# Performance work log

Measured on AMD Instinct MI355X. Metric: run time of the kernel, lower is better.

Reference implementation:

```python
import jax, jax.numpy as jnp
import numpy as np

T, D, H, FF, L = 4096, 512, 8, 2048, 6  # tokens, model dim, heads, ffn hidden, shared layers
HW = D // H  # head width = 64
N_SEG = 8
EPS = 1e-12


def setup_inputs() -> dict:
    key = jax.random.key(0)
    ks = jax.random.split(key, 16)
    s = 0.02

    def w(k, shape):
        return (jax.random.normal(k, shape, jnp.float32) * s)

    return {
        "h": jax.random.normal(ks[0], (T, D), jnp.float32),
        "seg_ids": jnp.sort(jax.random.randint(ks[1], (T,), 0, N_SEG, jnp.int32)),
        # attention projections (shared across layers, as in the torch module)
        "Wq": w(ks[2], (D, D)), "bq": jnp.zeros((D,), jnp.float32),
        "Wk": w(ks[3], (D, D)), "bk": jnp.zeros((D,), jnp.float32),
        "Wv": w(ks[4], (D, D)), "bv": jnp.zeros((D,), jnp.float32),
        "Wc": w(ks[5], (D, D)), "bc": jnp.zeros((D,), jnp.float32),
        # output projection
        "Wp": w(ks[6], (D, D)), "bp": jnp.zeros((D,), jnp.float32),
        # layer norms
        "g1": jnp.ones((D,), jnp.float32), "b1": jnp.zeros((D,), jnp.float32),
        "g2": jnp.ones((D,), jnp.float32), "b2": jnp.zeros((D,), jnp.float32),
        # position-wise FFN
        "W1": w(ks[7], (D, FF)), "fb1": jnp.zeros((FF,), jnp.float32),
        "W2": w(ks[8], (FF, D)), "fb2": jnp.zeros((D,), jnp.float32),
    }


def _layernorm(x, gamma, beta):
    # TF-style LN: eps inside the sqrt, biased variance
    u = x.mean(-1, keepdims=True)
    s = ((x - u) ** 2).mean(-1, keepdims=True)
    return gamma * (x - u) / jnp.sqrt(s + EPS) + beta


def _swish(x):
    return x * jax.nn.sigmoid(x)


def reference(h, seg_ids, Wq, bq, Wk, bk, Wv, bv, Wc, bc, Wp, bp,
              g1, b1, g2, b2, W1, fb1, W2, fb2):
    # Segment-local attention: equivalent to the torch per-split loop, since
    # softmax over a block-diagonal mask == per-segment softmax.
    mask = seg_ids[:, None] == seg_ids[None, :]  # [T, T]
    scale = 1.0 / np.sqrt(HW).astype(np.float32)
    for _ in range(L):  # shared weights across layers, as in the module
        prev = h
        q = (h @ Wq + bq).reshape(T, H, HW)
        k = (h @ Wk + bk).reshape(T, H, HW)
        v = (h @ Wv + bv).reshape(T, H, HW)
        c = h @ Wc + bc
        scores = jnp.einsum("thw,shw->hts", q, k) * scale  # [H, T, T]
        scores = jnp.where(mask[None], scores, jnp.float32(-1e30))
        att = jax.nn.softmax(scores, axis=-1)
        attn_out = jnp.einsum("hts,shw->thw", att, v).reshape(T, D) + c
        h = _layernorm(prev + attn_out @ Wp + bp, g1, b1)
        h = _layernorm(h + _swish(h @ W1 + fb1) @ W2 + fb2, g2, b2)
    return h
```

## Files before the change

### kernel.cpp

```cpp
#include <hip/hip_runtime.h>
#include <stdint.h>

#define TTOK 4096
#define DMODEL 512
#define NHEAD 8
#define FFDIM 2048
#define NLAYER 6

typedef short bf16x8 __attribute__((ext_vector_type(8)));
typedef float f32x4 __attribute__((ext_vector_type(4)));

__device__ __forceinline__ unsigned short f2bf(float f) {
  union { float f; unsigned int u; } v; v.f = f;
  unsigned int u = v.u;
  unsigned int r = (u + 0x7FFFu + ((u >> 16) & 1u)) >> 16;
  return (unsigned short)r;
}

__device__ __forceinline__ float bf2f(unsigned short h) {
  union { unsigned int u; float f; } v; v.u = ((unsigned int)h) << 16;
  return v.f;
}

#define GLOAD_LDS16(gp, lp)                                                      \
  __builtin_amdgcn_global_load_lds(                                              \
      (const __attribute__((address_space(1))) unsigned int*)(gp),               \
      (__attribute__((address_space(3))) unsigned int*)(lp), 16, 0, 0)

__global__ void transpose_cast(const float* __restrict__ src, unsigned short* __restrict__ dst,
                               int K, int N) {
  __shared__ float tile[32][33];
  const int n0 = blockIdx.x * 32, k0 = blockIdx.y * 32;
  const int x = threadIdx.x, y = threadIdx.y;
#pragma unroll
  for (int yy = 0; yy < 32; yy += 8)
    tile[y + yy][x] = src[(size_t)(k0 + y + yy) * N + n0 + x];
  __syncthreads();
#pragma unroll
  for (int yy = 0; yy < 32; yy += 8)
    dst[(size_t)(n0 + y + yy) * K + k0 + x] = f2bf(tile[x][y + yy]);
}

__global__ void pack_bias(const float* __restrict__ bq, const float* __restrict__ bk,
                          const float* __restrict__ bv, const float* __restrict__ bc,
                          float* __restrict__ out) {
  int i = blockIdx.x * 256 + threadIdx.x;
  const float* src = (i < 512) ? bq : (i < 1024) ? bk : (i < 1536) ? bv : bc;
  out[i] = src[i & 511];
}

__global__ void cast_bf16(const float* __restrict__ src, unsigned short* __restrict__ dst, int n4) {
  int i = blockIdx.x * 256 + threadIdx.x;
  if (i < n4) {
    float4 v = ((const float4*)src)[i];
    uint2 o;
    o.x = (unsigned int)f2bf(v.x) | ((unsigned int)f2bf(v.y) << 16);
    o.y = (unsigned int)f2bf(v.z) | ((unsigned int)f2bf(v.w) << 16);
    ((uint2*)dst)[i] = o;
  }
}

__global__ void seg_bounds(const int* __restrict__ seg, int* __restrict__ ss,
                           int* __restrict__ se, int T) {
  const int t = blockIdx.x * 256 + threadIdx.x;
  if (t >= T) return;
  const int sid = seg[t];
  int lo = 0, hi = T;
  while (lo < hi) { int mid = (lo + hi) >> 1; if (seg[mid] < sid) lo = mid + 1; else hi = mid; }
  ss[t] = lo;
  lo = t; hi = T;
  while (lo < hi) { int mid = (lo + hi) >> 1; if (seg[mid] <= sid) lo = mid + 1; else hi = mid; }
  se[t] = lo;
}

template <int MODE, int MF>
__launch_bounds__(256)
__global__ void gemm_bf16(const unsigned short* __restrict__ A,
                          const unsigned short* __restrict__ Bt,
                          int M, int N, int K,
                          const float* __restrict__ bias,
                          const float* __restrict__ res,
                          float* __restrict__ outF,
                          unsigned short* __restrict__ outB) {
  __shared__ uint4 As[MF * 256];
  __shared__ uint4 Bs[1024];
  const int tid = threadIdx.x;
  const int lane = tid & 63;
  const int wv = tid >> 6;
  const int wm = wv >> 1, wn = wv & 1;
  const int l15 = lane & 15, l4 = lane >> 4;
  const int bm0 = blockIdx.x * (MF * 32);
  const int bn0 = blockIdx.y * 128;

  f32x4 acc[MF][4];
#pragma unroll
  for (int m = 0; m < MF; ++m)
#pragma unroll
    for (int n = 0; n < 4; ++n) acc[m][n] = (f32x4){0.f, 0.f, 0.f, 0.f};

  for (int k0 = 0; k0 < K; k0 += 64) {
#pragma unroll
    for (int i = 0; i < MF; ++i) {
      const int u = tid + i * 256;
      const int r = u >> 3;
      const int c = (u & 7) ^ (r & 7);
      GLOAD_LDS16(A + (size_t)(bm0 + r) * K + k0 + c * 8, &As[i * 256 + wv * 64]);
    }
#pragma unroll
    for (int i = 0; i < 4; ++i) {
      const int u = tid + i * 256;
      const int r = u >> 3;
      const int c = (u & 7) ^ (r & 7);
      GLOAD_LDS16(Bt + (size_t)(bn0 + r) * K + k0 + c * 8, &Bs[i * 256 + wv * 64]);
    }
    __syncthreads();
#pragma unroll
    for (int kk = 0; kk < 2; ++kk) {
      bf16x8 af[MF], bfr[4];
#pragma unroll
      for (int m = 0; m < MF; ++m) {
        const int row = wm * (MF * 16) + m * 16 + l15;
        const int c = kk * 4 + l4;
        af[m] = *(const bf16x8*)&As[row * 8 + (c ^ (row & 7))];
      }
#pragma unroll
      for (int n = 0; n < 4; ++n) {
        const int row = wn * 64 + n * 16 + l15;
        const int c = kk * 4 + l4;
        bfr[n] = *(const bf16x8*)&Bs[row * 8 + (c ^ (row & 7))];
      }
#pragma unroll
      for (int m = 0; m < MF; ++m)
#pragma unroll
        for (int n = 0; n < 4; ++n)
          acc[m][n] = __builtin_amdgcn_mfma_f32_16x16x32_bf16(af[m], bfr[n], acc[m][n], 0, 0, 0);
    }
    __syncthreads();
  }

  float bvals[4];
#pragma unroll
  for (int n = 0; n < 4; ++n) bvals[n] = bias[bn0 + wn * 64 + n * 16 + l15];

#pragma unroll
  for (int m = 0; m < MF; ++m) {
#pragma unroll
    for (int r = 0; r < 4; ++r) {
      const int R = bm0 + wm * (MF * 16) + m * 16 + l4 * 4 + r;
#pragma unroll
      for (int n = 0; n < 4; ++n) {
        const int C = bn0 + wn * 64 + n * 16 + l15;
        float v = acc[m][n][r] + bvals[n];
        if (MODE == 1) {
          v += res[(size_t)R * N + C];
          outF[(size_t)R * N + C] = v;
        } else if (MODE == 2) {
          v = v / (1.f + __expf(-v));
          outB[(size_t)R * N + C] = f2bf(v);
        } else {
          outB[(size_t)R * N + C] = f2bf(v);
        }
      }
    }
  }
}

__launch_bounds__(64)
__global__ void attn_mfma(const unsigned short* __restrict__ qkvcb,
                          const int* __restrict__ sstart,
                          const int* __restrict__ send,
                          unsigned short* __restrict__ aob) {
  __shared__ unsigned short Vt[64 * 68];
  __shared__ unsigned short Pl[16 * 68];
  const int lane = threadIdx.x;
  const int l15 = lane & 15;
  const int g = lane >> 4;
  const int head = blockIdx.x & 7;
  const int q0 = (blockIdx.x >> 3) * 16;

  const size_t qbase = (size_t)(q0 + l15) * 2048 + head * 64;
  const bf16x8 qf0 = *(const bf16x8*)(qkvcb + qbase + g * 8);
  const bf16x8 qf1 = *(const bf16x8*)(qkvcb + qbase + 32 + g * 8);

  int sr[4], er[4];
#pragma unroll
  for (int r = 0; r < 4; ++r) {
    const int q = q0 + 4 * g + r;
    sr[r] = sstart[q];
    er[r] = send[q];
  }
  const int s0 = sstart[q0];
  const int e1 = send[q0 + 15];

  uint4 vreg[8];
  bf16x8 kfa[4], kfb[4];

  auto LOADV = [&](int k0) {
    const unsigned short* vrow =
        qkvcb + (size_t)min(k0 + lane, TTOK - 1) * 2048 + 1024 + head * 64;
#pragma unroll
    for (int d8 = 0; d8 < 8; ++d8) vreg[d8] = *(const uint4*)(vrow + d8 * 8);
  };
  auto LOADK = [&](int k0) {
#pragma unroll
    for (int n = 0; n < 4; ++n) {
      const size_t kb =
          (size_t)min(k0 + 16 * n + l15, TTOK - 1) * 2048 + 512 + head * 64;
      kfa[n] = *(const bf16x8*)(qkvcb + kb + g * 8);
      kfb[n] = *(const bf16x8*)(qkvcb + kb + 32 + g * 8);
    }
  };
  LOADV(s0);
  LOADK(s0);

  float m_[4], l_[4];
  f32x4 o[4];
#pragma unroll
  for (int r = 0; r < 4; ++r) { m_[r] = -1e30f; l_[r] = 0.f; }
#pragma unroll
  for (int n = 0; n < 4; ++n) o[n] = (f32x4){0.f, 0.f, 0.f, 0.f};

  for (int k0 = s0; k0 < e1; k0 += 64) {
#pragma unroll
    for (int d8 = 0; d8 < 8; ++d8) {
      const unsigned int uu[4] = {vreg[d8].x, vreg[d8].y, vreg[d8].z, vreg[d8].w};
#pragma unroll
      for (int t2 = 0; t2 < 4; ++t2) {
        Vt[(d8 * 8 + 2 * t2) * 68 + lane] = (unsigned short)(uu[t2] & 0xFFFFu);
        Vt[(d8 * 8 + 2 * t2 + 1) * 68 + lane] = (unsigned short)(uu[t2] >> 16);
      }
    }

    f32x4 sac[4];
#pragma unroll
    for (int n = 0; n < 4; ++n) {
      f32x4 z = (f32x4){0.f, 0.f, 0.f, 0.f};
      z = __builtin_amdgcn_mfma_f32_16x16x32_bf16(qf0, kfa[n], z, 0, 0, 0);
      sac[n] = __builtin_amdgcn_mfma_f32_16x16x32_bf16(qf1, kfb[n], z, 0, 0, 0);
    }

    const int k0n = (k0 + 64 < e1) ? (k0 + 64) : s0;
    LOADV(k0n);
    LOADK(k0n);

    float pv[4][4];
    float pmax[4] = {-1e30f, -1e30f, -1e30f, -1e30f};
#pragma unroll
    for (int n = 0; n < 4; ++n) {
      const int col = k0 + 16 * n + l15;
#pragma unroll
      for (int r = 0; r < 4; ++r) {
        float v = sac[n][r] * 0.125f;
        if (col < sr[r] || col >= er[r]) v = -1e30f;
        pv[n][r] = v;
        pmax[r] = fmaxf(pmax[r], v);
      }
    }
    bool need = false;
#pragma unroll
    for (int r = 0; r < 4; ++r) need |= (pmax[r] > m_[r] + 8.f);
    if (__any(need)) {
      float tm[4];
#pragma unroll
      for (int r = 0; r < 4; ++r) tm[r] = pmax[r];
#pragma unroll
      for (int off = 1; off < 16; off <<= 1) {
#pragma unroll
        for (int r = 0; r < 4; ++r) tm[r] = fmaxf(tm[r], __shfl_xor(tm[r], off));
      }
      f32x4 corrv;
#pragma unroll
      for (int r = 0; r < 4; ++r) {
        const float nm = fmaxf(m_[r], tm[r]);
        const float corr = __expf(m_[r] - nm);
        m_[r] = nm;
        l_[r] *= corr;
        corrv[r] = corr;
      }
#pragma unroll
      for (int n = 0; n < 4; ++n) o[n] *= corrv;
    }
    float psum[4] = {0.f, 0.f, 0.f, 0.f};
#pragma unroll
    for (int n = 0; n < 4; ++n) {
#pragma unroll
      for (int r = 0; r < 4; ++r) {
        const float p = __expf(pv[n][r] - m_[r]);
        pv[n][r] = p;
        psum[r] += p;
      }
    }
#pragma unroll
    for (int off = 1; off < 16; off <<= 1) {
#pragma unroll
      for (int r = 0; r < 4; ++r) psum[r] += __shfl_xor(psum[r], off);
    }
#pragma unroll
    for (int r = 0; r < 4; ++r) l_[r] += psum[r];

#pragma unroll
    for (int n = 0; n < 4; ++n)
#pragma unroll
      for (int r = 0; r < 4; ++r)
        Pl[(4 * g + r) * 68 + 16 * n + l15] = f2bf(pv[n][r]);

    const bf16x8 pa0 = *(const bf16x8*)(Pl + l15 * 68 + g * 8);
    const bf16x8 pa1 = *(const bf16x8*)(Pl + l15 * 68 + 32 + g * 8);
#pragma unroll
    for (int n = 0; n < 4; ++n) {
      const bf16x8 vb0 = *(const bf16x8*)(Vt + (16 * n + l15) * 68 + g * 8);
      const bf16x8 vb1 = *(const bf16x8*)(Vt + (16 * n + l15) * 68 + 32 + g * 8);
      o[n] = __builtin_amdgcn_mfma_f32_16x16x32_bf16(pa0, vb0, o[n], 0, 0, 0);
      o[n] = __builtin_amdgcn_mfma_f32_16x16x32_bf16(pa1, vb1, o[n], 0, 0, 0);
    }
  }

  float rl[4];
#pragma unroll
  for (int r = 0; r < 4; ++r) rl[r] = 1.f / l_[r];
#pragma unroll
  for (int n = 0; n < 4; ++n) {
#pragma unroll
    for (int r = 0; r < 4; ++r) {
      const int q = q0 + 4 * g + r;
      const int d = head * 64 + 16 * n + l15;
      const float cv = bf2f(qkvcb[(size_t)q * 2048 + 1536 + d]);
      aob[(size_t)q * 512 + d] = f2bf(o[n][r] * rl[r] + cv);
    }
  }
}

__launch_bounds__(64)
__global__ void ln_kernel(const float* __restrict__ x, const float* __restrict__ g,
                          const float* __restrict__ b, float* __restrict__ outF,
                          unsigned short* __restrict__ outB) {
  const int row = blockIdx.x;
  const int lane = threadIdx.x;
  const float4* xr = (const float4*)(x + (size_t)row * 512);
  float4 a = xr[lane * 2], c = xr[lane * 2 + 1];
  float s = a.x + a.y + a.z + a.w + c.x + c.y + c.z + c.w;
  float sq = a.x * a.x + a.y * a.y + a.z * a.z + a.w * a.w +
             c.x * c.x + c.y * c.y + c.z * c.z + c.w * c.w;
#pragma unroll
  for (int off = 1; off < 64; off <<= 1) {
    s += __shfl_xor(s, off);
    sq += __shfl_xor(sq, off);
  }
  const float mean = s * (1.f / 512.f);
  const float var = sq * (1.f / 512.f) - mean * mean;
  const float rstd = rsqrtf(var + 1e-12f);
  const float4* gr = (const float4*)g;
  const float4* br = (const float4*)b;
  float4 g0 = gr[lane * 2], g1v = gr[lane * 2 + 1];
  float4 b0 = br[lane * 2], b1v = br[lane * 2 + 1];
  float4 y0, y1;
  y0.x = (a.x - mean) * rstd * g0.x + b0.x;
  y0.y = (a.y - mean) * rstd * g0.y + b0.y;
  y0.z = (a.z - mean) * rstd * g0.z + b0.z;
  y0.w = (a.w - mean) * rstd * g0.w + b0.w;
  y1.x = (c.x - mean) * rstd * g1v.x + b1v.x;
  y1.y = (c.y - mean) * rstd * g1v.y + b1v.y;
  y1.z = (c.z - mean) * rstd * g1v.z + b1v.z;
  y1.w = (c.w - mean) * rstd * g1v.w + b1v.w;
  float4* of = (float4*)(outF + (size_t)row * 512);
  of[lane * 2] = y0;
  of[lane * 2 + 1] = y1;
  uint4 ob;
  ob.x = (unsigned int)f2bf(y0.x) | ((unsigned int)f2bf(y0.y) << 16);
  ob.y = (unsigned int)f2bf(y0.z) | ((unsigned int)f2bf(y0.w) << 16);
  ob.z = (unsigned int)f2bf(y1.x) | ((unsigned int)f2bf(y1.y) << 16);
  ob.w = (unsigned int)f2bf(y1.z) | ((unsigned int)f2bf(y1.w) << 16);
  ((uint4*)(outB + (size_t)row * 512))[lane] = ob;
}

extern "C" void kernel_launch(void* const* d_in, const int* in_sizes, int n_in,
                              void* d_out, int out_size, void* d_ws, size_t ws_size,
                              hipStream_t stream) {
  const float* h_in = (const float*)d_in[0];
  const int* seg = (const int*)d_in[1];
  const float* Wq = (const float*)d_in[2];
  const float* bq = (const float*)d_in[3];
  const float* Wk = (const float*)d_in[4];
  const float* bk = (const float*)d_in[5];
  const float* Wv = (const float*)d_in[6];
  const float* bv = (const float*)d_in[7];
  const float* Wc = (const float*)d_in[8];
  const float* bc = (const float*)d_in[9];
  const float* Wp = (const float*)d_in[10];
  const float* bp = (const float*)d_in[11];
  const float* g1 = (const float*)d_in[12];
  const float* b1 = (const float*)d_in[13];
  const float* g2 = (const float*)d_in[14];
  const float* b2 = (const float*)d_in[15];
  const float* W1 = (const float*)d_in[16];
  const float* fb1 = (const float*)d_in[17];
  const float* W2 = (const float*)d_in[18];
  const float* fb2 = (const float*)d_in[19];
  float* outp = (float*)d_out;

  char* p = (char*)d_ws;
  auto alloc = [&](size_t bytes) {
    char* r = p;
    p += (bytes + 255) & ~(size_t)255;
    return r;
  };
  unsigned short* wqkvcb = (unsigned short*)alloc((size_t)2048 * 512 * 2);
  unsigned short* wpb = (unsigned short*)alloc((size_t)512 * 512 * 2);
  unsigned short* w1b = (unsigned short*)alloc((size_t)2048 * 512 * 2);
  unsigned short* w2b = (unsigned short*)alloc((size_t)512 * 2048 * 2);
  float* bqkvc = (float*)alloc(2048 * 4);
  unsigned short* hb = (unsigned short*)alloc((size_t)TTOK * 512 * 2);
  unsigned short* qkvcb = (unsigned short*)alloc((size_t)TTOK * 2048 * 2);
  unsigned short* aob = (unsigned short*)alloc((size_t)TTOK * 512 * 2);
  float* xbuf = (float*)alloc((size_t)TTOK * 512 * 4);
  float* h1 = (float*)alloc((size_t)TTOK * 512 * 4);
  unsigned short* h1b = (unsigned short*)alloc((size_t)TTOK * 512 * 2);
  unsigned short* f1b = (unsigned short*)alloc((size_t)TTOK * 2048 * 2);
  float* hcur = (float*)alloc((size_t)TTOK * 512 * 4);
  int* sstart = (int*)alloc(TTOK * 4);
  int* send = (int*)alloc(TTOK * 4);

  dim3 tb(32, 8);
  transpose_cast<<<dim3(16, 16), tb, 0, stream>>>(Wq, wqkvcb + 0 * 512 * 512, 512, 512);
  transpose_cast<<<dim3(16, 16), tb, 0, stream>>>(Wk, wqkvcb + 1 * 512 * 512, 512, 512);
  transpose_cast<<<dim3(16, 16), tb, 0, stream>>>(Wv, wqkvcb + 2 * 512 * 512, 512, 512);
  transpose_cast<<<dim3(16, 16), tb, 0, stream>>>(Wc, wqkvcb + 3 * 512 * 512, 512, 512);
  transpose_cast<<<dim3(16, 16), tb, 0, stream>>>(Wp, wpb, 512, 512);
  transpose_cast<<<dim3(64, 16), tb, 0, stream>>>(W1, w1b, 512, 2048);
  transpose_cast<<<dim3(16, 64), tb, 0, stream>>>(W2, w2b, 2048, 512);
  pack_bias<<<8, 256, 0, stream>>>(bq, bk, bv, bc, bqkvc);
  cast_bf16<<<2048, 256, 0, stream>>>(h_in, hb, TTOK * 512 / 4);
  seg_bounds<<<16, 256, 0, stream>>>(seg, sstart, send, TTOK);

  const float* resp = h_in;
  for (int layer = 0; layer < NLAYER; ++layer) {
    gemm_bf16<0, 4><<<dim3(32, 16), 256, 0, stream>>>(hb, wqkvcb, TTOK, 2048, 512,
                                                      bqkvc, nullptr, nullptr, qkvcb);
    attn_mfma<<<dim3(2048), 64, 0, stream>>>(qkvcb, sstart, send, aob);
    gemm_bf16<1, 2><<<dim3(64, 4), 256, 0, stream>>>(aob, wpb, TTOK, 512, 512,
                                                     bp, resp, xbuf, nullptr);
    ln_kernel<<<TTOK, 64, 0, stream>>>(xbuf, g1, b1, h1, h1b);
    gemm_bf16<2, 4><<<dim3(32, 16), 256, 0, stream>>>(h1b, w1b, TTOK, 2048, 512,
                                                      fb1, nullptr, nullptr, f1b);
    gemm_bf16<1, 2><<<dim3(64, 4), 256, 0, stream>>>(f1b, w2b, TTOK, 512, 2048,
                                                     fb2, h1, xbuf, nullptr);
    float* lnout = (layer == NLAYER - 1) ? outp : hcur;
    ln_kernel<<<TTOK, 64, 0, stream>>>(xbuf, g2, b2, lnout, hb);
    resp = hcur;
  }
}
```

Measured before the change: 843.2 us.

## Split attention key range across four waves per block with LDS merge

The attention kernel now launches 256 threads per block. Each of the four waves handles every fourth 64-key chunk of the segment and keeps its own running max, sum and output. At the end the waves write their partial softmax state into LDS, reusing their V tile buffers, and wave 0 merges them with exp-rescaling before adding the c term and writing the bf16 output. This shortens the serial key loop per query tile and adds more waves in flight to hide load latency. The cost is four times the LDS per block, a block-wide barrier, and a serial merge done by one wave.

```diff
diff --git a/kernel.cpp b/kernel.cpp
--- a/kernel.cpp
+++ b/kernel.cpp
@@ -165,18 +165,22 @@
   }
 }
 
-__launch_bounds__(64)
+__launch_bounds__(256)
 __global__ void attn_mfma(const unsigned short* __restrict__ qkvcb,
                           const int* __restrict__ sstart,
                           const int* __restrict__ send,
                           unsigned short* __restrict__ aob) {
-  __shared__ unsigned short Vt[64 * 68];
-  __shared__ unsigned short Pl[16 * 68];
-  const int lane = threadIdx.x;
+  __shared__ unsigned short VtAll[4 * 64 * 68];
+  __shared__ unsigned short PlAll[4 * 16 * 68];
+  const int tid = threadIdx.x;
+  const int lane = tid & 63;
+  const int wq = tid >> 6;
   const int l15 = lane & 15;
   const int g = lane >> 4;
   const int head = blockIdx.x & 7;
   const int q0 = (blockIdx.x >> 3) * 16;
+  unsigned short* Vt = &VtAll[wq * 64 * 68];
+  unsigned short* Pl = &PlAll[wq * 16 * 68];
 
   const size_t qbase = (size_t)(q0 + l15) * 2048 + head * 64;
   const bf16x8 qf0 = *(const bf16x8*)(qkvcb + qbase + g * 8);
@@ -210,8 +214,9 @@
       kfb[n] = *(const bf16x8*)(qkvcb + kb + 32 + g * 8);
     }
   };
-  LOADV(s0);
-  LOADK(s0);
+  const int kstart = s0 + wq * 64;
+  LOADV(kstart);
+  LOADK(kstart);
 
   float m_[4], l_[4];
   f32x4 o[4];
@@ -220,7 +225,7 @@
 #pragma unroll
   for (int n = 0; n < 4; ++n) o[n] = (f32x4){0.f, 0.f, 0.f, 0.f};
 
-  for (int k0 = s0; k0 < e1; k0 += 64) {
+  for (int k0 = kstart; k0 < e1; k0 += 256) {
 #pragma unroll
     for (int d8 = 0; d8 < 8; ++d8) {
       const unsigned int uu[4] = {vreg[d8].x, vreg[d8].y, vreg[d8].z, vreg[d8].w};
@@ -239,7 +244,7 @@
       sac[n] = __builtin_amdgcn_mfma_f32_16x16x32_bf16(qf1, kfb[n], z, 0, 0, 0);
     }
 
-    const int k0n = (k0 + 64 < e1) ? (k0 + 64) : s0;
+    const int k0n = (k0 + 256 < e1) ? (k0 + 256) : s0;
     LOADV(k0n);
     LOADK(k0n);
 
@@ -315,17 +320,62 @@
     }
   }
 
-  float rl[4];
-#pragma unroll
-  for (int r = 0; r < 4; ++r) rl[r] = 1.f / l_[r];
-#pragma unroll
-  for (int n = 0; n < 4; ++n) {
+  {
+    float* slab = (float*)Vt;
+    const int base = lane * 25;
+#pragma unroll
+    for (int n = 0; n < 4; ++n)
+#pragma unroll
+      for (int r = 0; r < 4; ++r) slab[base + 4 * n + r] = o[n][r];
 #pragma unroll
     for (int r = 0; r < 4; ++r) {
-      const int q = q0 + 4 * g + r;
-      const int d = head * 64 + 16 * n + l15;
-      const float cv = bf2f(qkvcb[(size_t)q * 2048 + 1536 + d]);
-      aob[(size_t)q * 512 + d] = f2bf(o[n][r] * rl[r] + cv);
+      slab[base + 16 + r] = m_[r];
+      slab[base + 20 + r] = l_[r];
+    }
+  }
+  __syncthreads();
+
+  if (wq == 0) {
+    const int base = lane * 25;
+    float M[4];
+#pragma unroll
+    for (int r = 0; r < 4; ++r) M[r] = -1e30f;
+#pragma unroll
+    for (int w = 0; w < 4; ++w) {
+      const float* sw = (const float*)&VtAll[w * 64 * 68];
+#pragma unroll
+      for (int r = 0; r < 4; ++r) M[r] = fmaxf(M[r], sw[base + 16 + r]);
+    }
+    float L[4] = {0.f, 0.f, 0.f, 0.f};
+    f32x4 O[4];
+#pragma unroll
+    for (int n = 0; n < 4; ++n) O[n] = (f32x4){0.f, 0.f, 0.f, 0.f};
+#pragma unroll
+    for (int w = 0; w < 4; ++w) {
+      const float* sw = (const float*)&VtAll[w * 64 * 68];
+      float wgt[4];
+#pragma unroll
+      for (int r = 0; r < 4; ++r) {
+        wgt[r] = __expf(sw[base + 16 + r] - M[r]);
+        L[r] += sw[base + 20 + r] * wgt[r];
+      }
+#pragma unroll
+      for (int n = 0; n < 4; ++n)
+#pragma unroll
+        for (int r = 0; r < 4; ++r) O[n][r] += sw[base + 4 * n + r] * wgt[r];
+    }
+    float rl[4];
+#pragma unroll
+    for (int r = 0; r < 4; ++r) rl[r] = 1.f / L[r];
+#pragma unroll
+    for (int n = 0; n < 4; ++n) {
+#pragma unroll
+      for (int r = 0; r < 4; ++r) {
+        const int q = q0 + 4 * g + r;
+        const int d = head * 64 + 16 * n + l15;
+        const float cv = bf2f(qkvcb[(size_t)q * 2048 + 1536 + d]);
+        aob[(size_t)q * 512 + d] = f2bf(O[n][r] * rl[r] + cv);
+      }
     }
   }
 }
@@ -436,7 +486,7 @@
   for (int layer = 0; layer < NLAYER; ++layer) {
     gemm_bf16<0, 4><<<dim3(32, 16), 256, 0, stream>>>(hb, wqkvcb, TTOK, 2048, 512,
                                                       bqkvc, nullptr, nullptr, qkvcb);
-    attn_mfma<<<dim3(2048), 64, 0, stream>>>(qkvcb, sstart, send, aob);
+    attn_mfma<<<dim3(2048), 256, 0, stream>>>(qkvcb, sstart, send, aob);
     gemm_bf16<1, 2><<<dim3(64, 4), 256, 0, stream>>>(aob, wpb, TTOK, 512, 512,
                                                      bp, resp, xbuf, nullptr);
     ln_kernel<<<TTOK, 64, 0, stream>>>(xbuf, g1, b1, h1, h1b);
```

Result: slower. 936.5 us (+11.1%).

## Stage V via async global-to-LDS loads with double buffer and transpose reads

Applied to the files above, without the earlier changes.

Replaces the register-staged V load and scalar transposed LDS stores in the attention kernel with direct global_load_lds transfers into a double-buffered LDS tile. The PV matmul operands are then read with ds_read_b64_tr_b16 transpose reads. This removes the many 16-bit LDS writes and VGPRs used for V staging and overlaps the next tile's V fetch with compute. It relies on inline asm with an explicit waitcnt, and no visible wait on the async global-to-LDS loads, so there is a correctness or hazard risk. It also doubles LDS use.

```diff
diff --git a/kernel.cpp b/kernel.cpp
--- a/kernel.cpp
+++ b/kernel.cpp
@@ -9,6 +9,7 @@
 
 typedef short bf16x8 __attribute__((ext_vector_type(8)));
 typedef float f32x4 __attribute__((ext_vector_type(4)));
+typedef int v2i __attribute__((ext_vector_type(2)));
 
 __device__ __forceinline__ unsigned short f2bf(float f) {
   union { float f; unsigned int u; } v; v.f = f;
@@ -170,7 +171,7 @@
                           const int* __restrict__ sstart,
                           const int* __restrict__ send,
                           unsigned short* __restrict__ aob) {
-  __shared__ unsigned short Vt[64 * 68];
+  __shared__ unsigned short Vt[2 * 4096];
   __shared__ unsigned short Pl[16 * 68];
   const int lane = threadIdx.x;
   const int l15 = lane & 15;
@@ -192,15 +193,10 @@
   const int s0 = sstart[q0];
   const int e1 = send[q0 + 15];
 
-  uint4 vreg[8];
+  const int vtokrel = lane >> 1;
+  const unsigned short* vsrc = qkvcb + 1024 + head * 64 + (lane & 1) * 8;
+
   bf16x8 kfa[4], kfb[4];
-
-  auto LOADV = [&](int k0) {
-    const unsigned short* vrow =
-        qkvcb + (size_t)min(k0 + lane, TTOK - 1) * 2048 + 1024 + head * 64;
-#pragma unroll
-    for (int d8 = 0; d8 < 8; ++d8) vreg[d8] = *(const uint4*)(vrow + d8 * 8);
-  };
   auto LOADK = [&](int k0) {
 #pragma unroll
     for (int n = 0; n < 4; ++n) {
@@ -210,7 +206,16 @@
       kfb[n] = *(const bf16x8*)(qkvcb + kb + 32 + g * 8);
     }
   };
-  LOADV(s0);
+  auto STAGEV = [&](int k0, int buf) {
+#pragma unroll
+    for (int i = 0; i < 8; ++i) {
+      const int tok = min(k0 + vtokrel + (i & 1) * 32, TTOK - 1);
+      GLOAD_LDS16(vsrc + (size_t)tok * 2048 + (i >> 1) * 16,
+                  Vt + buf * 4096 + i * 512);
+    }
+  };
+
+  STAGEV(s0, 0);
   LOADK(s0);
 
   float m_[4], l_[4];
@@ -220,17 +225,8 @@
 #pragma unroll
   for (int n = 0; n < 4; ++n) o[n] = (f32x4){0.f, 0.f, 0.f, 0.f};
 
+  int buf = 0;
   for (int k0 = s0; k0 < e1; k0 += 64) {
-#pragma unroll
-    for (int d8 = 0; d8 < 8; ++d8) {
-      const unsigned int uu[4] = {vreg[d8].x, vreg[d8].y, vreg[d8].z, vreg[d8].w};
-#pragma unroll
-      for (int t2 = 0; t2 < 4; ++t2) {
-        Vt[(d8 * 8 + 2 * t2) * 68 + lane] = (unsigned short)(uu[t2] & 0xFFFFu);
-        Vt[(d8 * 8 + 2 * t2 + 1) * 68 + lane] = (unsigned short)(uu[t2] >> 16);
-      }
-    }
-
     f32x4 sac[4];
 #pragma unroll
     for (int n = 0; n < 4; ++n) {
@@ -240,7 +236,7 @@
     }
 
     const int k0n = (k0 + 64 < e1) ? (k0 + 64) : s0;
-    LOADV(k0n);
+    STAGEV(k0n, buf ^ 1);
     LOADK(k0n);
 
     float pv[4][4];
@@ -303,16 +299,43 @@
 #pragma unroll
       for (int r = 0; r < 4; ++r)
         Pl[(4 * g + r) * 68 + 16 * n + l15] = f2bf(pv[n][r]);
-
     const bf16x8 pa0 = *(const bf16x8*)(Pl + l15 * 68 + g * 8);
     const bf16x8 pa1 = *(const bf16x8*)(Pl + l15 * 68 + 32 + g * 8);
-#pragma unroll
-    for (int n = 0; n < 4; ++n) {
-      const bf16x8 vb0 = *(const bf16x8*)(Vt + (16 * n + l15) * 68 + g * 8);
-      const bf16x8 vb1 = *(const bf16x8*)(Vt + (16 * n + l15) * 68 + 32 + g * 8);
-      o[n] = __builtin_amdgcn_mfma_f32_16x16x32_bf16(pa0, vb0, o[n], 0, 0, 0);
-      o[n] = __builtin_amdgcn_mfma_f32_16x16x32_bf16(pa1, vb1, o[n], 0, 0, 0);
-    }
+
+    {
+      const __attribute__((address_space(3))) unsigned short* vb3 =
+          ((const __attribute__((address_space(3))) unsigned short*)Vt) +
+          buf * 4096 + g * 128 + l15 * 4;
+      v2i t[16];
+      asm volatile("ds_read_b64_tr_b16 %0, %1"              : "=v"(t[0])  : "v"(vb3));
+      asm volatile("ds_read_b64_tr_b16 %0, %1 offset:128"   : "=v"(t[1])  : "v"(vb3));
+      asm volatile("ds_read_b64_tr_b16 %0, %1 offset:1024"  : "=v"(t[2])  : "v"(vb3));
+      asm volatile("ds_read_b64_tr_b16 %0, %1 offset:1152"  : "=v"(t[3])  : "v"(vb3));
+      asm volatile("ds_read_b64_tr_b16 %0, %1 offset:2048"  : "=v"(t[4])  : "v"(vb3));
+      asm volatile("ds_read_b64_tr_b16 %0, %1 offset:2176"  : "=v"(t[5])  : "v"(vb3));
+      asm volatile("ds_read_b64_tr_b16 %0, %1 offset:3072"  : "=v"(t[6])  : "v"(vb3));
+      asm volatile("ds_read_b64_tr_b16 %0, %1 offset:3200"  : "=v"(t[7])  : "v"(vb3));
+      asm volatile("ds_read_b64_tr_b16 %0, %1 offset:4096"  : "=v"(t[8])  : "v"(vb3));
+      asm volatile("ds_read_b64_tr_b16 %0, %1 offset:4224"  : "=v"(t[9])  : "v"(vb3));
+      asm volatile("ds_read_b64_tr_b16 %0, %1 offset:5120"  : "=v"(t[10]) : "v"(vb3));
+      asm volatile("ds_read_b64_tr_b16 %0, %1 offset:5248"  : "=v"(t[11]) : "v"(vb3));
+      asm volatile("ds_read_b64_tr_b16 %0, %1 offset:6144"  : "=v"(t[12]) : "v"(vb3));
+      asm volatile("ds_read_b64_tr_b16 %0, %1 offset:6272"  : "=v"(t[13]) : "v"(vb3));
+      asm volatile("ds_read_b64_tr_b16 %0, %1 offset:7168"  : "=v"(t[14]) : "v"(vb3));
+      asm volatile("ds_read_b64_tr_b16 %0, %1 offset:7296"  : "=v"(t[15]) : "v"(vb3));
+      asm volatile("s_waitcnt lgkmcnt(0)" ::: "memory");
+      __builtin_amdgcn_sched_barrier(0);
+      union VU { v2i p[2]; bf16x8 f; };
+#pragma unroll
+      for (int n = 0; n < 4; ++n) {
+        VU u0, u1;
+        u0.p[0] = t[4 * n];     u0.p[1] = t[4 * n + 1];
+        u1.p[0] = t[4 * n + 2]; u1.p[1] = t[4 * n + 3];
+        o[n] = __builtin_amdgcn_mfma_f32_16x16x32_bf16(pa0, u0.f, o[n], 0, 0, 0);
+        o[n] = __builtin_amdgcn_mfma_f32_16x16x32_bf16(pa1, u1.f, o[n], 0, 0, 0);
+      }
+    }
+    buf ^= 1;
   }
 
   float rl[4];
```

Result: faster. 815.4 us (-3.3%).
